# Performance work log

Measured on AMD Instinct MI355X. Metric: run time of the kernel, lower is better.

Reference implementation:

```python
import jax, jax.numpy as jnp
import numpy as np

LN_EPS = 1e-5
EPS = 1e-8
NUM_ITERS = 3

def _ln(x, w, b):
    mu = jnp.mean(x, axis=-1, keepdims=True)
    var = jnp.var(x, axis=-1, keepdims=True)
    return (x - mu) * jax.lax.rsqrt(var + LN_EPS) * w + b

def setup_inputs() -> dict:
    key = jax.random.key(0)
    ks = jax.random.split(key, 20)
    B, H, W, C = 16, 64, 64, 256
    D, S, HID, T = 128, 10, 256, 20
    g = lambda k, *shape: jax.random.normal(k, shape, dtype=jnp.float32) * 0.02
    return {
        'obs': jax.random.normal(ks[0], (B, H, W, C), dtype=jnp.float32),
        'noise': jax.random.normal(ks[1], (B, S, D), dtype=jnp.float32),
        'slots_mu': jax.random.normal(ks[2], (1, 1, D), dtype=jnp.float32),
        'slots_log_sigma': jax.random.normal(ks[3], (1, 1, D), dtype=jnp.float32) * 0.1,
        'ni_w': jnp.ones((C,), jnp.float32), 'ni_b': jnp.zeros((C,), jnp.float32),
        'ns_w': jnp.ones((D,), jnp.float32), 'ns_b': jnp.zeros((D,), jnp.float32),
        'nm_w': jnp.ones((D,), jnp.float32), 'nm_b': jnp.zeros((D,), jnp.float32),
        'Wq': g(ks[4], D, D), 'Wk': g(ks[5], C, D), 'Wv': g(ks[6], C, D),
        'mlp_w1': g(ks[7], D, 2 * D), 'mlp_b1': jnp.zeros((2 * D,), jnp.float32),
        'mlp_w2': g(ks[8], 2 * D, D), 'mlp_b2': jnp.zeros((D,), jnp.float32),
        'pd_w1': g(ks[9], D, HID), 'pd_b1': jnp.zeros((HID,), jnp.float32),
        'pd_w2': g(ks[10], HID, D), 'pd_b2': jnp.zeros((D,), jnp.float32),
        'tc_w': g(ks[11], D, T), 'tc_b': jnp.zeros((T,), jnp.float32),
    }

def reference(obs, noise, slots_mu, slots_log_sigma, ni_w, ni_b, ns_w, ns_b,
              nm_w, nm_b, Wq, Wk, Wv, mlp_w1, mlp_b1, mlp_w2, mlp_b2,
              pd_w1, pd_b1, pd_w2, pd_b2, tc_w, tc_b):
    B = obs.shape[0]
    x = obs.reshape(B, -1, obs.shape[-1])  # [B, N, C] (flatten H,W)
    D = Wq.shape[0]
    # slot init: mu + sigma * noise
    slots = slots_mu + jnp.exp(slots_log_sigma) * noise  # [B, S, D]
    x = _ln(x, ni_w, ni_b)
    k = x @ Wk  # [B, N, D]
    v = x @ Wv  # [B, N, D]
    scale = D ** -0.5
    attn = None
    for _ in range(NUM_ITERS):
        slots_prev = slots
        q = _ln(slots, ns_w, ns_b) @ Wq  # [B, S, D]
        logits = jnp.einsum('bsd,bnd->bsn', q, k) * scale
        attn = jax.nn.softmax(logits, axis=1)  # competitive over slots
        w = attn / (jnp.sum(attn, axis=-1, keepdims=True) + EPS)
        updates = jnp.einsum('bsn,bnd->bsd', w, v)
        slots = slots_prev + updates
        h = _ln(slots, nm_w, nm_b)
        slots = slots + (jax.nn.relu(h @ mlp_w1 + mlp_b1) @ mlp_w2 + mlp_b2)
    objects = jax.nn.relu(slots @ pd_w1 + pd_b1) @ pd_w2 + pd_b2
    object_types = slots @ tc_w + tc_b
    return objects, object_types
```

## Files before the change

kernel.cpp:

```cpp
#include <hip/hip_runtime.h>
#include <hip/hip_bf16.h>

typedef __hip_bfloat16 bf16;
typedef __attribute__((ext_vector_type(8))) short bf16x8;
typedef __attribute__((ext_vector_type(4))) float f32x4;

#define LN_EPS 1e-5f
#define ATT_EPS 1e-8f
#define QSCALE 0.08838834764831845f

__device__ __forceinline__ float bflo(unsigned u){ union{unsigned i;float f;}c; c.i=u<<16; return c.f; }
__device__ __forceinline__ float bfhi(unsigned u){ union{unsigned i;float f;}c; c.i=u&0xffff0000u; return c.f; }
__device__ __forceinline__ float bf2f(bf16 h){ return __bfloat162float(h); }
__device__ __forceinline__ unsigned f2bfbits(float f){
    bf16 h = __float2bfloat16(f);
    unsigned short s; __builtin_memcpy(&s, &h, 2);
    return (unsigned)s;
}
__device__ __forceinline__ int detect_isf(const void* niw){
    unsigned u0; __builtin_memcpy(&u0, niw, 4);
    return (u0 == 0x3F800000u) ? 1 : 0;
}

__device__ __forceinline__ float getv(const void* p, long i, int isf){
    if (isf) return ((const float*)p)[i];
    return bf2f(((const bf16*)p)[i]);
}
__device__ __forceinline__ void get8(const void* p, long i, int isf, float* o){
    if (isf){
        __builtin_memcpy(o, (const float*)p + i, 32);
    } else {
        unsigned u[4];
        __builtin_memcpy(u, (const bf16*)p + i, 16);
        o[0]=bflo(u[0]); o[1]=bfhi(u[0]); o[2]=bflo(u[1]); o[3]=bfhi(u[1]);
        o[4]=bflo(u[2]); o[5]=bfhi(u[2]); o[6]=bflo(u[3]); o[7]=bfhi(u[3]);
    }
}
__device__ __forceinline__ void load4f(const float* p, float* o){ __builtin_memcpy(o, p, 16); }
__device__ __forceinline__ void store4f(float* p, const float* v){ __builtin_memcpy(p, v, 16); }

__device__ __forceinline__ void wred2(float& a, float& b){
    #pragma unroll
    for (int m = 32; m > 0; m >>= 1){
        a += __shfl_xor(a, m, 64);
        b += __shfl_xor(b, m, 64);
    }
}

__global__ __launch_bounds__(256) void k_prep_d(
        const void* __restrict__ noise, const void* __restrict__ smu,
        const void* __restrict__ sls, const void* __restrict__ nsw,
        const void* __restrict__ nsb, const void* __restrict__ niw,
        const void* __restrict__ nib, const void* __restrict__ Wq,
        const void* __restrict__ Wk, float* __restrict__ slots,
        bf16* __restrict__ wkqb, float* __restrict__ Ug, float* __restrict__ Vg,
        float* __restrict__ P2, float* __restrict__ t0g, float* __restrict__ t1g){
    int isf = detect_isf(niw);
    int bs = blockIdx.x, t = threadIdx.x;
    int b = bs/10, s = bs - b*10;
    __shared__ __align__(16) float shlns[128];
    __shared__ __align__(16) float sq2[2][128];
    __shared__ __align__(16) float qv[128];
    __shared__ float red[2][2];
    __shared__ float redUV[8];
    int wid = t >> 6, lane = t & 63;

    if (t < 128){
        float sv = getv(smu,t,isf) + __expf(getv(sls,t,isf)) * getv(noise,(long)bs*128+t,isf);
        slots[bs*128 + t] = sv;
        shlns[t] = sv;
        float su = sv, sqv = sv*sv;
        wred2(su, sqv);
        if (lane == 0){ red[wid][0]=su; red[wid][1]=sqv; }
    }
    __syncthreads();
    if (t < 128){
        float su = red[0][0]+red[1][0], sqv = red[0][1]+red[1][1];
        float m = su*(1.f/128.f), var = sqv*(1.f/128.f) - m*m;
        float ri = rsqrtf(var + LN_EPS);
        shlns[t] = (shlns[t] - m)*ri*getv(nsw,t,isf) + getv(nsb,t,isf);
    }
    __syncthreads();
    {
        int d = t & 127, half = t >> 7;
        float a = 0.f;
        #pragma unroll 8
        for (int dp = half*64; dp < half*64 + 64; dp++)
            a += shlns[dp]*getv(Wq, (long)dp*128 + d, isf);
        sq2[half][d] = a;
    }
    __syncthreads();
    if (t < 128) qv[t] = (sq2[0][t] + sq2[1][t]) * QSCALE;
    __syncthreads();
    {
        float kqc = 0.f;
        #pragma unroll
        for (int ch = 0; ch < 16; ch++){
            float w8[8]; get8(Wk, (long)t*128 + ch*8, isf, w8);
            #pragma unroll
            for (int j=0;j<8;j++) kqc += qv[ch*8+j]*w8[j];
        }
        float wc = getv(niw,t,isf), bc = getv(nib,t,isf);
        float wkq = wc*kqc, vq = bc*kqc;
        float uu = wkq, vv = vq;
        wred2(uu, vv);
        if (lane == 0){ redUV[wid*2] = uu; redUV[wid*2+1] = vv; }
        wkqb[((long)b*16 + s)*256 + t] = __float2bfloat16(wkq);
        P2[bs*256 + t] = 0.f;
        __syncthreads();
        if (t == 0){
            Ug[bs] = redUV[0] + redUV[2] + redUV[4] + redUV[6];
            Vg[bs] = redUV[1] + redUV[3] + redUV[5] + redUV[7];
            t0g[bs] = 0.f; t1g[bs] = 0.f;
        }
    }
    if (s == 0){
        #pragma unroll
        for (int r = 10; r < 16; r++)
            wkqb[((long)b*16 + r)*256 + t] = __float2bfloat16(0.f);
    }
}

__global__ __launch_bounds__(256) void k_attn5(
        const void* __restrict__ obs, const bf16* __restrict__ wkqb,
        const float* __restrict__ Ug, const float* __restrict__ Vg,
        const void* __restrict__ niw, float* __restrict__ P2,
        float* __restrict__ t0g, float* __restrict__ t1g){
    int isf = detect_isf(niw);
    int tile = blockIdx.x, b = blockIdx.y, t = threadIdx.x;
    int w = t >> 6, l = t & 63;
    __shared__ unsigned sxn[64*132];
    __shared__ __align__(16) float attnP[64*12];
    __shared__ float muri[128];
    __shared__ float denp0[4][16], denp1[4][16];

    if (isf){
        const float* gx = (const float*)obs + ((long)b*4096 + tile*64)*256;
        #pragma unroll
        for (int i = 0; i < 8; i++){
            int Ld = t*4 + i*1024;
            int px = Ld >> 7, col = Ld & 127;
            float f8[8];
            __builtin_memcpy(f8, gx + (long)px*256 + col*2, 32);
            unsigned pk[4];
            #pragma unroll
            for (int k2=0;k2<4;k2++)
                pk[k2] = (f2bfbits(f8[2*k2+1])<<16) | f2bfbits(f8[2*k2]);
            __builtin_memcpy(&sxn[px*132 + col], pk, 16);
        }
    } else {
        const unsigned* gx = (const unsigned*)obs + ((long)b*4096 + tile*64)*128;
        #pragma unroll
        for (int i = 0; i < 8; i++){
            int Ld = t*4 + i*1024;
            int px = Ld >> 7, col = Ld & 127;
            unsigned tmp[4];
            __builtin_memcpy(tmp, gx + Ld, 16);
            __builtin_memcpy(&sxn[px*132 + col], tmp, 16);
        }
    }
    bf16x8 bfr[8];
    {
        int s = l & 15, q = (l >> 4) & 3;
        const bf16* base = wkqb + ((long)b*16 + s)*256 + q*8;
        #pragma unroll
        for (int ks = 0; ks < 8; ks++)
            __builtin_memcpy(&bfr[ks], base + ks*32, 16);
    }
    __syncthreads();

    {
        int px = t >> 2, q = t & 3;
        float su = 0.f, sq = 0.f;
        #pragma unroll
        for (int j = 0; j < 8; j++){
            unsigned d4[4];
            __builtin_memcpy(d4, &sxn[px*132 + q*32 + j*4], 16);
            #pragma unroll
            for (int k2=0;k2<4;k2++){
                float a0 = bflo(d4[k2]), a1 = bfhi(d4[k2]);
                su += a0 + a1; sq += a0*a0 + a1*a1;
            }
        }
        su += __shfl_xor(su,1,64); sq += __shfl_xor(sq,1,64);
        su += __shfl_xor(su,2,64); sq += __shfl_xor(sq,2,64);
        if (q == 0){
            float m = su*(1.f/256.f);
            float ri = rsqrtf(sq*(1.f/256.f) - m*m + LN_EPS);
            muri[px*2] = m; muri[px*2+1] = ri;
        }
    }
    __syncthreads();

    f32x4 acc = {0.f,0.f,0.f,0.f};
    {
        int m = l & 15, q = (l >> 4) & 3;
        int rowbase = (w*16 + m)*132;
        #pragma unroll
        for (int ks = 0; ks < 8; ks++){
            bf16x8 af;
            __builtin_memcpy(&af, &sxn[rowbase + ks*16 + q*4], 16);
            acc = __builtin_amdgcn_mfma_f32_16x16x32_bf16(af, bfr[ks], acc, 0, 0, 0);
        }
    }

    {
        int col = l & 15, q = (l >> 4) & 3;
        float Uv = 0.f, Vv = 0.f;
        if (col < 10){ Uv = Ug[b*10 + col]; Vv = Vg[b*10 + col]; }
        float pden0 = 0.f, pden1 = 0.f;
        #pragma unroll
        for (int reg = 0; reg < 4; reg++){
            int px = w*16 + q*4 + reg;
            float mr[2]; __builtin_memcpy(mr, &muri[px*2], 8);
            float lg = (col < 10) ? (mr[1]*acc[reg] - mr[1]*mr[0]*Uv + Vv) : -1e30f;
            float mx = lg;
            mx = fmaxf(mx, __shfl_xor(mx,1,64));
            mx = fmaxf(mx, __shfl_xor(mx,2,64));
            mx = fmaxf(mx, __shfl_xor(mx,4,64));
            mx = fmaxf(mx, __shfl_xor(mx,8,64));
            float e = (col < 10) ? __expf(lg - mx) : 0.f;
            float sm = e;
            sm += __shfl_xor(sm,1,64);
            sm += __shfl_xor(sm,2,64);
            sm += __shfl_xor(sm,4,64);
            sm += __shfl_xor(sm,8,64);
            float a = e / sm;
            if (col < 10) attnP[px*12 + col] = a*mr[1];
            pden0 += a;
            pden1 += a*mr[1]*mr[0];
        }
        pden0 += __shfl_xor(pden0,16,64); pden0 += __shfl_xor(pden0,32,64);
        pden1 += __shfl_xor(pden1,16,64); pden1 += __shfl_xor(pden1,32,64);
        if (l < 10){ denp0[w][l] = pden0; denp1[w][l] = pden1; }
    }
    __syncthreads();
    if (t < 10){
        atomicAdd(&t0g[b*10 + t], denp0[0][t]+denp0[1][t]+denp0[2][t]+denp0[3][t]);
        atomicAdd(&t1g[b*10 + t], denp1[0][t]+denp1[1][t]+denp1[2][t]+denp1[3][t]);
    }

    {
        int c = t, ch = c >> 1, hh = c & 1;
        float pacc[10];
        #pragma unroll
        for (int s=0;s<10;s++) pacc[s]=0.f;
        for (int n = 0; n < 64; n++){
            unsigned d = sxn[n*132 + ch];
            float xv = hh ? bfhi(d) : bflo(d);
            float a[10];
            load4f(&attnP[n*12], a);
            load4f(&attnP[n*12 + 4], a + 4);
            __builtin_memcpy(a + 8, &attnP[n*12 + 8], 8);
            #pragma unroll
            for (int s=0;s<10;s++) pacc[s] += a[s]*xv;
        }
        #pragma unroll
        for (int s=0;s<10;s++) atomicAdd(&P2[b*2560 + s*256 + c], pacc[s]);
    }
}

__global__ __launch_bounds__(256) void k_slot3(
        float* __restrict__ slots, float* __restrict__ P2,
        float* __restrict__ t0g, float* __restrict__ t1g,
        const void* __restrict__ Wv,
        const void* __restrict__ nmw, const void* __restrict__ nmb,
        const void* __restrict__ w1, const void* __restrict__ b1,
        const void* __restrict__ w2, const void* __restrict__ b2,
        const void* __restrict__ nsw, const void* __restrict__ nsb,
        const void* __restrict__ niw, const void* __restrict__ nib,
        const void* __restrict__ pw1, const void* __restrict__ pb1,
        const void* __restrict__ pw2, const void* __restrict__ pb2,
        const void* __restrict__ tw, const void* __restrict__ tb,
        const void* __restrict__ Wq, const void* __restrict__ Wk,
        bf16* __restrict__ wkqb, float* __restrict__ Ug, float* __restrict__ Vg,
        void* __restrict__ out, int last){
    int isf = detect_isf(niw);
    int bs = blockIdx.x, t = threadIdx.x;
    int b = bs/10, s = bs - b*10;
    __shared__ __align__(16) float pr[256];
    __shared__ __align__(16) float redA[16*128];
    __shared__ __align__(16) float redB[8*256];
    __shared__ __align__(16) float redT[8*32];
    __shared__ __align__(16) float hld[128];
    __shared__ __align__(16) float hid[256];
    __shared__ __align__(16) float shlns[128];
    __shared__ float red[4][2];
    __shared__ float redUV[8];

    float t0v = t0g[bs], t1v = t1g[bs];
    float wc = getv(niw,t,isf), bcv = getv(nib,t,isf);
    pr[t] = (P2[bs*256 + t] - t1v)*wc + t0v*bcv;
    __syncthreads();

    {
        int g = t & 15, ks = t >> 4;
        int d0 = g*8;
        float a8[8] = {0,0,0,0,0,0,0,0};
        #pragma unroll
        for (int j=0;j<16;j++){
            int c2 = ks*16 + j;
            float w8[8]; get8(Wv, (long)c2*128 + d0, isf, w8);
            float pv = pr[c2];
            #pragma unroll
            for (int k=0;k<8;k++) a8[k] += pv*w8[k];
        }
        store4f(&redA[ks*128 + d0], a8);
        store4f(&redA[ks*128 + d0 + 4], a8+4);
    }
    __syncthreads();
    float dv = t0v + ATT_EPS;
    float sn = 0.f;
    if (t < 128){
        float u = 0.f;
        #pragma unroll
        for (int ks=0;ks<16;ks++) u += redA[ks*128 + t];
        sn = slots[bs*128 + t] + u/dv;
    }
    float v = (t < 128) ? sn : 0.f;
    float su = v, sq = v*v;
    wred2(su, sq);
    int wid = t >> 6, lane = t & 63;
    if (lane == 0){ red[wid][0]=su; red[wid][1]=sq; }
    __syncthreads();
    su = red[0][0]+red[1][0]+red[2][0]+red[3][0];
    sq = red[0][1]+red[1][1]+red[2][1]+red[3][1];
    float mu = su*(1.f/128.f), var = sq*(1.f/128.f) - mu*mu;
    float rinv = rsqrtf(var + LN_EPS);
    if (t < 128) hld[t] = (v-mu)*rinv*getv(nmw,t,isf) + getv(nmb,t,isf);
    __syncthreads();

    {
        int g = t & 31, ks = t >> 5;
        int h0 = g*8;
        float a8[8] = {0,0,0,0,0,0,0,0};
        #pragma unroll
        for (int j=0;j<16;j++){
            int d = ks*16 + j;
            float w8[8]; get8(w1, (long)d*256 + h0, isf, w8);
            float hv = hld[d];
            #pragma unroll
            for (int k=0;k<8;k++) a8[k] += hv*w8[k];
        }
        store4f(&redB[ks*256 + h0], a8);
        store4f(&redB[ks*256 + h0 + 4], a8+4);
    }
    __syncthreads();
    {
        float hb = getv(b1,t,isf);
        #pragma unroll
        for (int ks=0;ks<8;ks++) hb += redB[ks*256 + t];
        hid[t] = fmaxf(hb, 0.f);
    }
    __syncthreads();
    {
        int g = t & 15, ks = t >> 4;
        int d0 = g*8;
        float a8[8] = {0,0,0,0,0,0,0,0};
        #pragma unroll
        for (int j=0;j<16;j++){
            int h = ks*16 + j;
            float w8[8]; get8(w2, (long)h*128 + d0, isf, w8);
            float hv = hid[h];
            #pragma unroll
            for (int k=0;k<8;k++) a8[k] += hv*w8[k];
        }
        store4f(&redA[ks*128 + d0], a8);
        store4f(&redA[ks*128 + d0 + 4], a8+4);
    }
    __syncthreads();
    float v2 = 0.f;
    if (t < 128){
        float o = getv(b2,t,isf);
        #pragma unroll
        for (int ks=0;ks<16;ks++) o += redA[ks*128 + t];
        v2 = sn + o;
    }

    if (!last){
        if (t < 128) slots[bs*128 + t] = v2;
        float s2 = v2, ss2 = v2*v2;
        wred2(s2, ss2);
        if (lane == 0){ red[wid][0]=s2; red[wid][1]=ss2; }
        __syncthreads();
        s2 = red[0][0]+red[1][0]+red[2][0]+red[3][0];
        ss2 = red[0][1]+red[1][1]+red[2][1]+red[3][1];
        float mu2 = s2*(1.f/128.f), var2 = ss2*(1.f/128.f) - mu2*mu2;
        float ri2 = rsqrtf(var2 + LN_EPS);
        if (t < 128)
            shlns[t] = (v2 - mu2)*ri2*getv(nsw,t,isf) + getv(nsb,t,isf);
        __syncthreads();
        {
            int d = t & 127, half = t >> 7;
            float a = 0.f;
            #pragma unroll 8
            for (int dp = half*64; dp < half*64 + 64; dp++)
                a += shlns[dp]*getv(Wq, (long)dp*128 + d, isf);
            redA[half*128 + d] = a;
        }
        __syncthreads();
        if (t < 128) hld[t] = (redA[t] + redA[128 + t]) * QSCALE;
        __syncthreads();
        {
            float kqc = 0.f;
            #pragma unroll
            for (int ch = 0; ch < 16; ch++){
                float w8[8]; get8(Wk, (long)t*128 + ch*8, isf, w8);
                #pragma unroll
                for (int j=0;j<8;j++) kqc += hld[ch*8+j]*w8[j];
            }
            float wcc = getv(niw,t,isf), bcc = getv(nib,t,isf);
            float wkq = wcc*kqc, vq = bcc*kqc;
            float uu = wkq, vv = vq;
            wred2(uu, vv);
            if (lane == 0){ redUV[wid*2] = uu; redUV[wid*2+1] = vv; }
            wkqb[((long)b*16 + s)*256 + t] = __float2bfloat16(wkq);
            P2[bs*256 + t] = 0.f;
            __syncthreads();
            if (t == 0){
                Ug[bs] = redUV[0] + redUV[2] + redUV[4] + redUV[6];
                Vg[bs] = redUV[1] + redUV[3] + redUV[5] + redUV[7];
                t0g[bs] = 0.f; t1g[bs] = 0.f;
            }
        }
    } else {
        if (t < 128) shlns[t] = v2;
        __syncthreads();
        {
            int g = t & 31, ks = t >> 5;
            int h0 = g*8;
            float a8[8] = {0,0,0,0,0,0,0,0};
            #pragma unroll
            for (int j=0;j<16;j++){
                int d = ks*16 + j;
                float w8[8]; get8(pw1, (long)d*256 + h0, isf, w8);
                float hv = shlns[d];
                #pragma unroll
                for (int k=0;k<8;k++) a8[k] += hv*w8[k];
            }
            store4f(&redB[ks*256 + h0], a8);
            store4f(&redB[ks*256 + h0 + 4], a8+4);
        }
        __syncthreads();
        {
            float hb = getv(pb1,t,isf);
            #pragma unroll
            for (int ks=0;ks<8;ks++) hb += redB[ks*256 + t];
            hid[t] = fmaxf(hb, 0.f);
        }
        __syncthreads();
        {
            int g = t & 15, ks = t >> 4;
            int d0 = g*8;
            float a8[8] = {0,0,0,0,0,0,0,0};
            #pragma unroll
            for (int j=0;j<16;j++){
                int h = ks*16 + j;
                float w8[8]; get8(pw2, (long)h*128 + d0, isf, w8);
                float hv = hid[h];
                #pragma unroll
                for (int k=0;k<8;k++) a8[k] += hv*w8[k];
            }
            store4f(&redA[ks*128 + d0], a8);
            store4f(&redA[ks*128 + d0 + 4], a8+4);
        }
        {
            int ot = t & 31, ks = t >> 5;
            float a = 0.f;
            if (ot < 20){
                #pragma unroll
                for (int j=0;j<16;j++){
                    int d = ks*16 + j;
                    a += shlns[d]*getv(tw, (long)d*20 + ot, isf);
                }
            }
            redT[ks*32 + ot] = a;
        }
        __syncthreads();
        if (t < 128){
            float o = getv(pb2,t,isf);
            #pragma unroll
            for (int ks=0;ks<16;ks++) o += redA[ks*128 + t];
            int idx = bs*128 + t;
            if (isf) ((float*)out)[idx] = o; else ((bf16*)out)[idx] = __float2bfloat16(o);
        }
        if (t < 20){
            float o = getv(tb,t,isf);
            #pragma unroll
            for (int ks=0;ks<8;ks++) o += redT[ks*32 + t];
            int idx = 16*10*128 + bs*20 + t;
            if (isf) ((float*)out)[idx] = o; else ((bf16*)out)[idx] = __float2bfloat16(o);
        }
    }
}

extern "C" void kernel_launch(void* const* d_in, const int* in_sizes, int n_in,
                              void* d_out, int out_size, void* d_ws, size_t ws_size,
                              hipStream_t stream) {
    const void* obs   = d_in[0];
    const void* noise = d_in[1];
    const void* smu   = d_in[2];
    const void* sls   = d_in[3];
    const void* niw   = d_in[4];
    const void* nib   = d_in[5];
    const void* nsw   = d_in[6];
    const void* nsb   = d_in[7];
    const void* nmw   = d_in[8];
    const void* nmb   = d_in[9];
    const void* Wq    = d_in[10];
    const void* Wk    = d_in[11];
    const void* Wv    = d_in[12];
    const void* w1    = d_in[13];
    const void* b1    = d_in[14];
    const void* w2    = d_in[15];
    const void* b2    = d_in[16];
    const void* pw1   = d_in[17];
    const void* pb1   = d_in[18];
    const void* pw2   = d_in[19];
    const void* pb2   = d_in[20];
    const void* tw    = d_in[21];
    const void* tb    = d_in[22];

    char* ws = (char*)d_ws;
    float* t0g   = (float*)(ws + 1024);
    float* t1g   = (float*)(ws + 2048);
    float* Ug    = (float*)(ws + 3072);
    float* Vg    = (float*)(ws + 4096);
    float* slots = (float*)(ws + 5120);
    float* P2    = (float*)(ws + 87040);
    bf16*  wkqb  = (bf16*) (ws + 250880);

    k_prep_d<<<160, 256, 0, stream>>>(noise, smu, sls, nsw, nsb, niw, nib,
                                      Wq, Wk, slots, wkqb, Ug, Vg, P2, t0g, t1g);
    for (int it = 0; it < 3; it++){
        k_attn5<<<dim3(64, 16), 256, 0, stream>>>(obs, wkqb, Ug, Vg, niw, P2, t0g, t1g);
        k_slot3<<<160, 256, 0, stream>>>(slots, P2, t0g, t1g, Wv, nmw, nmb,
                                         w1, b1, w2, b2, nsw, nsb, niw, nib,
                                         pw1, pb1, pw2, pb2, tw, tb, Wq, Wk,
                                         wkqb, Ug, Vg, d_out, (it == 2) ? 1 : 0);
    }
}
```

Before: 251.2 us.

## Compute attention-weighted pixel sums with bf16 MFMA and per-tile partials instead of atomics

```diff
diff --git a/kernel.cpp b/kernel.cpp
--- a/kernel.cpp
+++ b/kernel.cpp
@@ -54,7 +54,7 @@
         const void* __restrict__ nib, const void* __restrict__ Wq,
         const void* __restrict__ Wk, float* __restrict__ slots,
         bf16* __restrict__ wkqb, float* __restrict__ Ug, float* __restrict__ Vg,
-        float* __restrict__ P2, float* __restrict__ t0g, float* __restrict__ t1g){
+        float* __restrict__ t0g, float* __restrict__ t1g){
     int isf = detect_isf(niw);
     int bs = blockIdx.x, t = threadIdx.x;
     int b = bs/10, s = bs - b*10;
@@ -106,7 +106,6 @@
         wred2(uu, vv);
         if (lane == 0){ redUV[wid*2] = uu; redUV[wid*2+1] = vv; }
         wkqb[((long)b*16 + s)*256 + t] = __float2bfloat16(wkq);
-        P2[bs*256 + t] = 0.f;
         __syncthreads();
         if (t == 0){
             Ug[bs] = redUV[0] + redUV[2] + redUV[4] + redUV[6];
@@ -121,18 +120,25 @@
     }
 }
 
-__global__ __launch_bounds__(256) void k_attn5(
+__global__ __launch_bounds__(256) void k_attn9(
         const void* __restrict__ obs, const bf16* __restrict__ wkqb,
         const float* __restrict__ Ug, const float* __restrict__ Vg,
-        const void* __restrict__ niw, float* __restrict__ P2,
+        const void* __restrict__ niw, float* __restrict__ P2p,
         float* __restrict__ t0g, float* __restrict__ t1g){
     int isf = detect_isf(niw);
     int tile = blockIdx.x, b = blockIdx.y, t = threadIdx.x;
     int w = t >> 6, l = t & 63;
     __shared__ unsigned sxn[64*132];
-    __shared__ __align__(16) float attnP[64*12];
+    __shared__ __align__(16) short sxT[256*72];
+    __shared__ __align__(16) short attnTh[16*72];
+    __shared__ __align__(16) short attnTl[16*72];
     __shared__ float muri[128];
     __shared__ float denp0[4][16], denp1[4][16];
+
+    if (t < 216){
+        ((unsigned*)attnTh)[360 + t] = 0u;
+        ((unsigned*)attnTl)[360 + t] = 0u;
+    }
 
     if (isf){
         const float* gx = (const float*)obs + ((long)b*4096 + tile*64)*256;
@@ -144,8 +150,12 @@
             __builtin_memcpy(f8, gx + (long)px*256 + col*2, 32);
             unsigned pk[4];
             #pragma unroll
-            for (int k2=0;k2<4;k2++)
-                pk[k2] = (f2bfbits(f8[2*k2+1])<<16) | f2bfbits(f8[2*k2]);
+            for (int k2=0;k2<4;k2++){
+                unsigned b0 = f2bfbits(f8[2*k2]), b1 = f2bfbits(f8[2*k2+1]);
+                pk[k2] = (b1 << 16) | b0;
+                sxT[(col*2 + 2*k2    )*72 + px] = (short)b0;
+                sxT[(col*2 + 2*k2 + 1)*72 + px] = (short)b1;
+            }
             __builtin_memcpy(&sxn[px*132 + col], pk, 16);
         }
     } else {
@@ -156,6 +166,11 @@
             int px = Ld >> 7, col = Ld & 127;
             unsigned tmp[4];
             __builtin_memcpy(tmp, gx + Ld, 16);
+            #pragma unroll
+            for (int k2=0;k2<4;k2++){
+                sxT[(col*2 + 2*k2    )*72 + px] = (short)(tmp[k2] & 0xffffu);
+                sxT[(col*2 + 2*k2 + 1)*72 + px] = (short)(tmp[k2] >> 16);
+            }
             __builtin_memcpy(&sxn[px*132 + col], tmp, 16);
         }
     }
@@ -226,7 +241,12 @@
             sm += __shfl_xor(sm,4,64);
             sm += __shfl_xor(sm,8,64);
             float a = e / sm;
-            if (col < 10) attnP[px*12 + col] = a*mr[1];
+            if (col < 10){
+                float ar = a*mr[1];
+                unsigned ah = f2bfbits(ar);
+                attnTh[col*72 + px] = (short)ah;
+                attnTl[col*72 + px] = (short)f2bfbits(ar - bflo(ah));
+            }
             pden0 += a;
             pden1 += a*mr[1]*mr[0];
         }
@@ -241,27 +261,35 @@
     }
 
     {
-        int c = t, ch = c >> 1, hh = c & 1;
-        float pacc[10];
-        #pragma unroll
-        for (int s=0;s<10;s++) pacc[s]=0.f;
-        for (int n = 0; n < 64; n++){
-            unsigned d = sxn[n*132 + ch];
-            float xv = hh ? bfhi(d) : bflo(d);
-            float a[10];
-            load4f(&attnP[n*12], a);
-            load4f(&attnP[n*12 + 4], a + 4);
-            __builtin_memcpy(a + 8, &attnP[n*12 + 8], 8);
-            #pragma unroll
-            for (int s=0;s<10;s++) pacc[s] += a[s]*xv;
-        }
-        #pragma unroll
-        for (int s=0;s<10;s++) atomicAdd(&P2[b*2560 + s*256 + c], pacc[s]);
+        int q = l >> 4, j = l & 15;
+        bf16x8 ah0, ah1, al0, al1;
+        __builtin_memcpy(&ah0, &attnTh[j*72 + q*8], 16);
+        __builtin_memcpy(&ah1, &attnTh[j*72 + 32 + q*8], 16);
+        __builtin_memcpy(&al0, &attnTl[j*72 + q*8], 16);
+        __builtin_memcpy(&al1, &attnTl[j*72 + 32 + q*8], 16);
+        #pragma unroll
+        for (int i = 0; i < 4; i++){
+            int c = w*64 + i*16 + j;
+            bf16x8 bx0, bx1;
+            __builtin_memcpy(&bx0, &sxT[c*72 + q*8], 16);
+            __builtin_memcpy(&bx1, &sxT[c*72 + 32 + q*8], 16);
+            f32x4 pa = {0.f,0.f,0.f,0.f};
+            pa = __builtin_amdgcn_mfma_f32_16x16x32_bf16(ah0, bx0, pa, 0,0,0);
+            pa = __builtin_amdgcn_mfma_f32_16x16x32_bf16(al0, bx0, pa, 0,0,0);
+            pa = __builtin_amdgcn_mfma_f32_16x16x32_bf16(ah1, bx1, pa, 0,0,0);
+            pa = __builtin_amdgcn_mfma_f32_16x16x32_bf16(al1, bx1, pa, 0,0,0);
+            #pragma unroll
+            for (int reg = 0; reg < 4; reg++){
+                int s = q*4 + reg;
+                if (s < 10)
+                    P2p[((long)(b*10 + s)*64 + tile)*256 + c] = pa[reg];
+            }
+        }
     }
 }
 
 __global__ __launch_bounds__(256) void k_slot3(
-        float* __restrict__ slots, float* __restrict__ P2,
+        float* __restrict__ slots, const float* __restrict__ P2p,
         float* __restrict__ t0g, float* __restrict__ t1g,
         const void* __restrict__ Wv,
         const void* __restrict__ nmw, const void* __restrict__ nmb,
@@ -290,7 +318,13 @@
 
     float t0v = t0g[bs], t1v = t1g[bs];
     float wc = getv(niw,t,isf), bcv = getv(nib,t,isf);
-    pr[t] = (P2[bs*256 + t] - t1v)*wc + t0v*bcv;
+    {
+        const float* pp = P2p + ((long)bs*64)*256 + t;
+        float u = 0.f;
+        #pragma unroll 8
+        for (int tl = 0; tl < 64; tl++) u += pp[tl*256];
+        pr[t] = (u - t1v)*wc + t0v*bcv;
+    }
     __syncthreads();
 
     {
@@ -415,7 +449,6 @@
             wred2(uu, vv);
             if (lane == 0){ redUV[wid*2] = uu; redUV[wid*2+1] = vv; }
             wkqb[((long)b*16 + s)*256 + t] = __float2bfloat16(wkq);
-            P2[bs*256 + t] = 0.f;
             __syncthreads();
             if (t == 0){
                 Ug[bs] = redUV[0] + redUV[2] + redUV[4] + redUV[6];
@@ -527,14 +560,14 @@
     float* Ug    = (float*)(ws + 3072);
     float* Vg    = (float*)(ws + 4096);
     float* slots = (float*)(ws + 5120);
-    float* P2    = (float*)(ws + 87040);
-    bf16*  wkqb  = (bf16*) (ws + 250880);
+    bf16*  wkqb  = (bf16*) (ws + 87040);
+    float* P2p   = (float*)(ws + 218112);
 
     k_prep_d<<<160, 256, 0, stream>>>(noise, smu, sls, nsw, nsb, niw, nib,
-                                      Wq, Wk, slots, wkqb, Ug, Vg, P2, t0g, t1g);
+                                      Wq, Wk, slots, wkqb, Ug, Vg, t0g, t1g);
     for (int it = 0; it < 3; it++){
-        k_attn5<<<dim3(64, 16), 256, 0, stream>>>(obs, wkqb, Ug, Vg, niw, P2, t0g, t1g);
-        k_slot3<<<160, 256, 0, stream>>>(slots, P2, t0g, t1g, Wv, nmw, nmb,
+        k_attn9<<<dim3(64, 16), 256, 0, stream>>>(obs, wkqb, Ug, Vg, niw, P2p, t0g, t1g);
+        k_slot3<<<160, 256, 0, stream>>>(slots, P2p, t0g, t1g, Wv, nmw, nmb,
                                          w1, b1, w2, b2, nsw, nsb, niw, nib,
                                          pw1, pb1, pw2, pb2, tw, tb, Wq, Wk,
                                          wkqb, Ug, Vg, d_out, (it == 2) ? 1 : 0);
```

Result: slower. 313.9 us (+25.0%).
